# Performance work log

Hardware: AMD Instinct MI355X
Metric: run time of the kernel (lower is better)

## Reference

```python
import jax, jax.numpy as jnp
import numpy as np

N_NODES = 50000
E_DIM = 128
H_DIM = 256
OUT_DIM = 2
N_EDGES = 800000
NEG_SLOPE = 0.01  # nn.LeakyReLU default


def gcn_conv(x, W, b, src, dst, n):
    """PyG GCNConv: h = x @ W; add self-loops; sym-normalized scatter-add; + bias."""
    h = x @ W  # [N, H]
    loop = jnp.arange(n, dtype=src.dtype)
    s = jnp.concatenate([src, loop])
    d = jnp.concatenate([dst, loop])
    w = jnp.ones_like(s, dtype=h.dtype)
    deg = jax.ops.segment_sum(w, d, num_segments=n)  # in-degree incl. self-loop
    dis = jnp.where(deg > 0, jax.lax.rsqrt(deg), jnp.zeros_like(deg))
    norm = dis[s] * dis[d]  # [E+N]
    msg = h[s] * norm[:, None]  # gather + scale
    out = jax.ops.segment_sum(msg, d, num_segments=n)  # scatter-add to targets
    return out + b


def setup_inputs() -> dict:
    key = jax.random.key(0)
    ks = jax.random.split(key, 12)
    inp = {
        "mask_feature": jax.random.normal(ks[0], (N_NODES, E_DIM), jnp.float32),
        "feature": jax.random.normal(ks[1], (N_NODES, E_DIM), jnp.float32),
        "edge_index": jax.random.randint(ks[2], (2, N_EDGES), 0, N_NODES, jnp.int64 if jax.config.jax_enable_x64 else jnp.int32),
        "edge_type": jax.random.randint(ks[3], (N_EDGES,), 0, 2, jnp.int64 if jax.config.jax_enable_x64 else jnp.int32),
        # learned parameters
        "W_in": jax.random.normal(ks[4], (E_DIM, H_DIM), jnp.float32) * 0.05,
        "b_in": jnp.zeros((H_DIM,), jnp.float32),
        "Wg1": jax.random.normal(ks[5], (H_DIM, H_DIM), jnp.float32) * 0.05,
        "bg1": jnp.zeros((H_DIM,), jnp.float32),
        "Wg2": jax.random.normal(ks[6], (H_DIM, H_DIM), jnp.float32) * 0.05,
        "bg2": jnp.zeros((H_DIM,), jnp.float32),
        "W_out": jax.random.normal(ks[7], (H_DIM, OUT_DIM), jnp.float32) * 0.05,
        "b_out": jnp.zeros((OUT_DIM,), jnp.float32),
    }
    return inp


def reference(mask_feature, feature, edge_index, edge_type,
              W_in, b_in, Wg1, bg1, Wg2, bg2, W_out, b_out):
    src, dst = edge_index[0], edge_index[1]
    n = mask_feature.shape[0]
    # main branch
    x = jax.nn.leaky_relu(mask_feature @ W_in + b_in, NEG_SLOPE)
    x = gcn_conv(x, Wg1, bg1, src, dst, n)
    # dropout is identity at inference
    x = gcn_conv(x, Wg2, bg2, src, dst, n)
    x = x @ W_out + b_out  # [N, out_dim]
    # mask branch
    m = jax.nn.leaky_relu((feature - mask_feature) @ W_in + b_in, NEG_SLOPE)
    m = m @ W_out + b_out  # [N, out_dim]
    return x * m
```

## Files before the change

kernel.cpp:

```cpp
#include <hip/hip_runtime.h>


#define NEG_SLOPE 0.01f
constexpr int HD = 256;
constexpr int CHUNK = 4096;
constexpr int BSTRIDE = 8192;

typedef __bf16 bf16x8 __attribute__((ext_vector_type(8)));
typedef unsigned short u16x8 __attribute__((ext_vector_type(8)));
typedef float f32x4 __attribute__((ext_vector_type(4)));

#define MFMA16 __builtin_amdgcn_mfma_f32_16x16x32_bf16

__device__ inline void split1(float v, unsigned short& h, unsigned short& l) {
  unsigned u = __float_as_uint(v);
  unsigned hb = u & 0xFFFF0000u;
  float lf = v - __uint_as_float(hb);
  unsigned ul = __float_as_uint(lf);
  h = (unsigned short)(hb >> 16);
  l = (unsigned short)((ul + 0x7FFFu + ((ul >> 16) & 1u)) >> 16);
}

__global__ __launch_bounds__(256) void k_prep(
    const float* __restrict__ Win, u16x8* __restrict__ Wf,
    const float* __restrict__ Wg1, const float* __restrict__ Wg2,
    const float* __restrict__ Wo, const float* __restrict__ bg1,
    const float* __restrict__ bg2, const float* __restrict__ bo,
    float* __restrict__ wb, float* __restrict__ uv, int* __restrict__ cur) {
  __shared__ float wt[256][2];
  const int bid = blockIdx.x, tid = threadIdx.x;
  if (bid < 32) {
    int f = bid * 4 + (tid >> 6);
    int lane = tid & 63;
    int nt = f >> 3, ks = (f >> 1) & 3, hl = f & 1;
    int n = nt * 16 + (lane & 15);
    int k0 = ks * 32 + (lane >> 4) * 8;
    u16x8 outv;
    #pragma unroll
    for (int j = 0; j < 8; ++j) {
      unsigned short h, l;
      split1(Win[(size_t)(k0 + j) * HD + n], h, l);
      outv[j] = hl ? l : h;
    }
    Wf[f * 64 + lane] = outv;
  } else if (bid == 32) {
    int r = tid;
    float s0 = 0.f, s1 = 0.f;
    for (int k = 0; k < 256; ++k) {
      float w = Wg2[r * 256 + k];
      s0 = fmaf(w, Wo[k * 2 + 0], s0);
      s1 = fmaf(w, Wo[k * 2 + 1], s1);
    }
    wt[r][0] = s0; wt[r][1] = s1;
    __syncthreads();
    float b0 = 0.f, b1 = 0.f;
    for (int k = 0; k < 256; ++k) {
      float w = Wg1[r * 256 + k];
      b0 = fmaf(w, wt[k][0], b0);
      b1 = fmaf(w, wt[k][1], b1);
    }
    wb[r * 2 + 0] = b0; wb[r * 2 + 1] = b1;
    if (r < 2) {
      float u = 0.f, v = 0.f;
      for (int k = 0; k < 256; ++k) {
        u = fmaf(bg1[k], wt[k][r], u);
        v = fmaf(bg2[k], Wo[k * 2 + r], v);
      }
      uv[r] = u;
      uv[2 + r] = v + bo[r];
    }
  } else {
    cur[tid] = 0;
  }
}

__global__ __launch_bounds__(256) void k_scatter(
    const int* __restrict__ src, const int* __restrict__ dst,
    int* __restrict__ cur, unsigned* __restrict__ packed, int E) {
  __shared__ int bins[256], lstart[256], gbase[256], lcur[256];
  __shared__ int wsum[4];
  __shared__ unsigned sbuf[CHUNK];
  const int t = threadIdx.x, b = blockIdx.x;
  const int lane = t & 63, wid = t >> 6;
  bins[t] = 0;
  __syncthreads();
  const int e0 = b * CHUNK, e1 = min(e0 + CHUNK, E), m = e1 - e0;
  for (int e = e0 + t; e < e1; e += 256)
    atomicAdd(&bins[dst[e] >> 8], 1);
  __syncthreads();
  {
    int v = bins[t], incl = v;
    #pragma unroll
    for (int o = 1; o < 64; o <<= 1) {
      int tmp = __shfl_up(incl, o, 64);
      if (lane >= o) incl += tmp;
    }
    if (lane == 63) wsum[wid] = incl;
    __syncthreads();
    int woff = 0;
    for (int w = 0; w < wid; ++w) woff += wsum[w];
    int st = woff + incl - v;
    lstart[t] = st;
    lcur[t] = st;
    gbase[t] = v ? atomicAdd(&cur[t], v) : 0;
  }
  __syncthreads();
  for (int e = e0 + t; e < e1; e += 256) {
    int d = dst[e], s = src[e];
    int slot = atomicAdd(&lcur[d >> 8], 1);
    sbuf[slot] = ((unsigned)d << 16) | (unsigned)s;
  }
  __syncthreads();
  for (int i = t; i < m; i += 256) {
    unsigned pv = sbuf[i];
    int bin = pv >> 24;
    packed[(size_t)bin * BSTRIDE + gbase[bin] + (i - lstart[bin])] = pv;
  }
}

__global__ __launch_bounds__(256) void k_p2(
    const unsigned* __restrict__ packed, const int* __restrict__ cur,
    int* __restrict__ rp, float4* __restrict__ q, int* __restrict__ csr, int N) {
  __shared__ int cnt[256], sc[256];
  __shared__ int wsum[4];
  __shared__ unsigned short sbuf[BSTRIDE];
  const int t = threadIdx.x;
  const int B = blockIdx.x;
  const int lane = t & 63, wid = t >> 6;
  int tot = cur[t], incl = tot;
  #pragma unroll
  for (int o = 1; o < 64; o <<= 1) {
    int tmp = __shfl_up(incl, o, 64);
    if (lane >= o) incl += tmp;
  }
  if (lane == 63) wsum[wid] = incl;
  __syncthreads();
  int woff = 0;
  for (int w = 0; w < wid; ++w) woff += wsum[w];
  sc[t] = woff + incl - tot;
  __syncthreads();
  const int base = sc[B];
  const int ecnt = cur[B];
  const unsigned* pk = packed + (size_t)B * BSTRIDE;
  cnt[t] = 0;
  __syncthreads();
  for (int i = t; i < ecnt; i += 256)
    atomicAdd(&cnt[(pk[i] >> 16) & 0xFF], 1);
  __syncthreads();
  int v = cnt[t];
  incl = v;
  #pragma unroll
  for (int o = 1; o < 64; o <<= 1) {
    int tmp = __shfl_up(incl, o, 64);
    if (lane >= o) incl += tmp;
  }
  if (lane == 63) wsum[wid] = incl;
  __syncthreads();
  woff = 0;
  for (int w = 0; w < wid; ++w) woff += wsum[w];
  const int off = woff + incl - v;
  const int node = B * 256 + t;
  if (node < N) {
    rp[node] = base + off;
    ((float*)&q[node])[0] = rsqrtf((float)(v + 1));
  } else if (node == N) {
    rp[N] = base + off;
  }
  __syncthreads();
  cnt[t] = off;
  __syncthreads();
  for (int i = t; i < ecnt; i += 256) {
    unsigned pv = pk[i];
    int slot = atomicAdd(&cnt[(pv >> 16) & 0xFF], 1);
    sbuf[slot] = (unsigned short)(pv & 0xFFFFu);
  }
  __syncthreads();
  for (int i = t; i < ecnt; i += 256)
    csr[base + i] = (int)sbuf[i];
}

__global__ __launch_bounds__(512, 2) void k_gemm(
    const float* __restrict__ mf, const float* __restrict__ fe,
    const u16x8* __restrict__ Wf, const float* __restrict__ bi,
    const float* __restrict__ wb, const float* __restrict__ Wo,
    const float* __restrict__ bo, float4* __restrict__ q,
    float* __restrict__ Pm, int M) {
  __shared__ u16x8 sWf[8192];
  const int tid = threadIdx.x;
  #pragma unroll
  for (int i = 0; i < 16; ++i) sWf[tid + i * 512] = Wf[tid + i * 512];
  const int lane = tid & 63, wid = tid >> 6;
  const int base = blockIdx.x * 256 + wid * 32;
  const int kb = (lane >> 4) * 8;

  bf16x8 ahi[2][4], alo[2][4], mhi[2][4], mlo[2][4];
  #pragma unroll
  for (int h = 0; h < 2; ++h) {
    int arow = base + h * 16 + (lane & 15);
    if (arow >= M) arow = M - 1;
    const float* ap = mf + (size_t)arow * 128 + kb;
    const float* fp = fe + (size_t)arow * 128 + kb;
    #pragma unroll
    for (int ks = 0; ks < 4; ++ks) {
      float x[8], y[8];
      *(float4*)&x[0] = *(const float4*)(ap + ks * 32);
      *(float4*)&x[4] = *(const float4*)(ap + ks * 32 + 4);
      *(float4*)&y[0] = *(const float4*)(fp + ks * 32);
      *(float4*)&y[4] = *(const float4*)(fp + ks * 32 + 4);
      u16x8 hA, lA, hM, lM;
      #pragma unroll
      for (int j = 0; j < 8; ++j) {
        unsigned short hh, ll;
        split1(x[j], hh, ll);        hA[j] = hh; lA[j] = ll;
        split1(y[j] - x[j], hh, ll); hM[j] = hh; lM[j] = ll;
      }
      ahi[h][ks] = __builtin_bit_cast(bf16x8, hA);
      alo[h][ks] = __builtin_bit_cast(bf16x8, lA);
      mhi[h][ks] = __builtin_bit_cast(bf16x8, hM);
      mlo[h][ks] = __builtin_bit_cast(bf16x8, lM);
    }
  }
  __syncthreads();

  float s0[2][4] = {}, s1[2][4] = {}, t0[2][4] = {}, t1[2][4] = {};
  #pragma unroll 1
  for (int nt = 0; nt < 16; ++nt) {
    f32x4 aM[2] = {{0,0,0,0},{0,0,0,0}}, aK[2] = {{0,0,0,0},{0,0,0,0}};
    #pragma unroll
    for (int ks = 0; ks < 4; ++ks) {
      bf16x8 bh = __builtin_bit_cast(bf16x8, sWf[(nt * 8 + ks * 2 + 0) * 64 + lane]);
      bf16x8 bl = __builtin_bit_cast(bf16x8, sWf[(nt * 8 + ks * 2 + 1) * 64 + lane]);
      #pragma unroll
      for (int h = 0; h < 2; ++h) {
        aM[h] = MFMA16(ahi[h][ks], bh, aM[h], 0, 0, 0);
        aM[h] = MFMA16(alo[h][ks], bh, aM[h], 0, 0, 0);
        aM[h] = MFMA16(ahi[h][ks], bl, aM[h], 0, 0, 0);
        aK[h] = MFMA16(mhi[h][ks], bh, aK[h], 0, 0, 0);
        aK[h] = MFMA16(mlo[h][ks], bh, aK[h], 0, 0, 0);
        aK[h] = MFMA16(mhi[h][ks], bl, aK[h], 0, 0, 0);
      }
    }
    const int col = nt * 16 + (lane & 15);
    const float bc = bi[col];
    const float w0 = wb[col * 2 + 0], w1 = wb[col * 2 + 1];
    const float v0 = Wo[col * 2 + 0], v1 = Wo[col * 2 + 1];
    #pragma unroll
    for (int h = 0; h < 2; ++h) {
      #pragma unroll
      for (int r = 0; r < 4; ++r) {
        float a = aM[h][r] + bc; a = a > 0.f ? a : NEG_SLOPE * a;
        s0[h][r] = fmaf(a, w0, s0[h][r]); s1[h][r] = fmaf(a, w1, s1[h][r]);
        float m = aK[h][r] + bc; m = m > 0.f ? m : NEG_SLOPE * m;
        t0[h][r] = fmaf(m, v0, t0[h][r]); t1[h][r] = fmaf(m, v1, t1[h][r]);
      }
    }
  }

  #pragma unroll
  for (int o = 1; o < 16; o <<= 1) {
    #pragma unroll
    for (int h = 0; h < 2; ++h) {
      #pragma unroll
      for (int r = 0; r < 4; ++r) {
        s0[h][r] += __shfl_xor(s0[h][r], o, 16);
        s1[h][r] += __shfl_xor(s1[h][r], o, 16);
        t0[h][r] += __shfl_xor(t0[h][r], o, 16);
        t1[h][r] += __shfl_xor(t1[h][r], o, 16);
      }
    }
  }
  if ((lane & 15) == 0) {
    float bo0 = bo[0], bo1 = bo[1];
    #pragma unroll
    for (int h = 0; h < 2; ++h) {
      #pragma unroll
      for (int r = 0; r < 4; ++r) {
        int row = base + h * 16 + (lane >> 4) * 4 + r;
        if (row < M) {
          float* qf = (float*)&q[row];
          qf[1] = s0[h][r];
          qf[2] = s1[h][r];
          Pm[row * 2 + 0] = t0[h][r] + bo0;
          Pm[row * 2 + 1] = t1[h][r] + bo1;
        }
      }
    }
  }
}

__global__ __launch_bounds__(256) void k_gather1(
    const int* __restrict__ rp, const int* __restrict__ csr,
    const float4* __restrict__ q, const float* __restrict__ uv,
    float* __restrict__ T2, int N) {
  int t = threadIdx.x;
  int n = blockIdx.x * 64 + (t >> 2);
  int l = t & 3;
  if (n >= N) return;
  int s0 = rp[n], s1 = rp[n + 1];
  float a0 = 0.f, a1 = 0.f;
  int j = s0 + l;
  for (; j + 4 < s1; j += 8) {
    int sa = csr[j], sb = csr[j + 4];
    float4 qa = q[sa], qb = q[sb];
    a0 = fmaf(qa.x, qa.y, a0); a1 = fmaf(qa.x, qa.z, a1);
    a0 = fmaf(qb.x, qb.y, a0); a1 = fmaf(qb.x, qb.z, a1);
  }
  if (j < s1) {
    float4 qa = q[csr[j]];
    a0 = fmaf(qa.x, qa.y, a0); a1 = fmaf(qa.x, qa.z, a1);
  }
  a0 += __shfl_xor(a0, 1, 4); a1 += __shfl_xor(a1, 1, 4);
  a0 += __shfl_xor(a0, 2, 4); a1 += __shfl_xor(a1, 2, 4);
  if (l == 0) {
    float4 qn = q[n];
    float d = qn.x;
    T2[n * 2 + 0] = d * (d * fmaf(d, qn.y, a0) + uv[0]);
    T2[n * 2 + 1] = d * (d * fmaf(d, qn.z, a1) + uv[1]);
  }
}

__global__ __launch_bounds__(256) void k_gather2(
    const int* __restrict__ rp, const int* __restrict__ csr,
    const float* __restrict__ T2, const float4* __restrict__ q,
    const float* __restrict__ uv, const float* __restrict__ Pm,
    float* __restrict__ out, int N) {
  int t = threadIdx.x;
  int n = blockIdx.x * 64 + (t >> 2);
  int l = t & 3;
  if (n >= N) return;
  int s0 = rp[n], s1 = rp[n + 1];
  float a0 = 0.f, a1 = 0.f;
  int j = s0 + l;
  for (; j + 4 < s1; j += 8) {
    int sa = csr[j], sb = csr[j + 4];
    float2 va = *(const float2*)&T2[sa * 2];
    float2 vb = *(const float2*)&T2[sb * 2];
    a0 += va.x + vb.x; a1 += va.y + vb.y;
  }
  if (j < s1) {
    float2 va = *(const float2*)&T2[csr[j] * 2];
    a0 += va.x; a1 += va.y;
  }
  a0 += __shfl_xor(a0, 1, 4); a1 += __shfl_xor(a1, 1, 4);
  a0 += __shfl_xor(a0, 2, 4); a1 += __shfl_xor(a1, 2, 4);
  if (l == 0) {
    float d = q[n].x;
    float2 tv = *(const float2*)&T2[n * 2];
    float z0 = d * (tv.x + a0) + uv[2];
    float z1 = d * (tv.y + a1) + uv[3];
    out[n * 2 + 0] = z0 * Pm[n * 2 + 0];
    out[n * 2 + 1] = z1 * Pm[n * 2 + 1];
  }
}

extern "C" void kernel_launch(void* const* d_in, const int* in_sizes, int n_in,
                              void* d_out, int out_size, void* d_ws, size_t ws_size,
                              hipStream_t stream) {
  const float* mf  = (const float*)d_in[0];
  const float* fe  = (const float*)d_in[1];
  const int*   ei  = (const int*)d_in[2];
  const float* Win = (const float*)d_in[4];
  const float* bin = (const float*)d_in[5];
  const float* Wg1 = (const float*)d_in[6];
  const float* bg1 = (const float*)d_in[7];
  const float* Wg2 = (const float*)d_in[8];
  const float* bg2 = (const float*)d_in[9];
  const float* Wo  = (const float*)d_in[10];
  const float* bo  = (const float*)d_in[11];
  float* out = (float*)d_out;

  const int ED = 128;
  const int N = in_sizes[0] / ED;
  const int E = in_sizes[3];
  const int* src = ei;
  const int* dst = ei + E;

  char* ws = (char*)d_ws;
  size_t off = 0;
  auto carve = [&](size_t bytes) {
    char* p = ws + off;
    off += (bytes + 255) & ~(size_t)255;
    return p;
  };
  int*      cur    = (int*)carve(256 * 4);
  unsigned* packed = (unsigned*)carve((size_t)256 * BSTRIDE * 4);
  int*      csr    = (int*)carve((size_t)E * 4);
  int*      rp     = (int*)carve((size_t)(N + 1) * 4);
  float4*   q      = (float4*)carve((size_t)N * 16);
  float*    T2     = (float*)carve((size_t)N * 2 * 4);
  float*    Pm     = (float*)carve((size_t)N * 2 * 4);
  float*    wb     = (float*)carve((size_t)HD * 2 * 4);
  float*    uv     = (float*)carve(4 * 4);
  u16x8*    Wf     = (u16x8*)carve((size_t)128 * 64 * 16);
  (void)ws_size; (void)n_in; (void)out_size;

  const int NB  = (E + CHUNK - 1) / CHUNK;
  const int NP2 = (N + 255) / 256;
  const int Gg  = (N + 255) / 256;
  const int Gt  = (N + 63) / 64;

  k_prep<<<34, 256, 0, stream>>>(Win, Wf, Wg1, Wg2, Wo, bg1, bg2, bo, wb, uv, cur);
  k_scatter<<<NB, 256, 0, stream>>>(src, dst, cur, packed, E);
  k_p2<<<NP2, 256, 0, stream>>>(packed, cur, rp, q, csr, N);
  k_gemm<<<Gg, 512, 0, stream>>>(mf, fe, Wf, bin, wb, Wo, bo, q, Pm, N);
  k_gather1<<<Gt, 256, 0, stream>>>(rp, csr, q, uv, T2, N);
  k_gather2<<<Gt, 256, 0, stream>>>(rp, csr, T2, q, uv, Pm, out, N);
}
```

Before: 100.8 us.

## Fuse CSR build and GEMM into one launch, stream weights in chunks, unroll gathers

Result: faster. 89.54 us (-11.2%).

```diff
diff --git a/kernel.cpp b/kernel.cpp
--- a/kernel.cpp
+++ b/kernel.cpp
@@ -118,88 +118,32 @@
   }
 }
 
-__global__ __launch_bounds__(256) void k_p2(
-    const unsigned* __restrict__ packed, const int* __restrict__ cur,
-    int* __restrict__ rp, float4* __restrict__ q, int* __restrict__ csr, int N) {
-  __shared__ int cnt[256], sc[256];
-  __shared__ int wsum[4];
-  __shared__ unsigned short sbuf[BSTRIDE];
-  const int t = threadIdx.x;
-  const int B = blockIdx.x;
-  const int lane = t & 63, wid = t >> 6;
-  int tot = cur[t], incl = tot;
-  #pragma unroll
-  for (int o = 1; o < 64; o <<= 1) {
-    int tmp = __shfl_up(incl, o, 64);
-    if (lane >= o) incl += tmp;
-  }
-  if (lane == 63) wsum[wid] = incl;
-  __syncthreads();
-  int woff = 0;
-  for (int w = 0; w < wid; ++w) woff += wsum[w];
-  sc[t] = woff + incl - tot;
-  __syncthreads();
-  const int base = sc[B];
-  const int ecnt = cur[B];
-  const unsigned* pk = packed + (size_t)B * BSTRIDE;
-  cnt[t] = 0;
-  __syncthreads();
-  for (int i = t; i < ecnt; i += 256)
-    atomicAdd(&cnt[(pk[i] >> 16) & 0xFF], 1);
-  __syncthreads();
-  int v = cnt[t];
-  incl = v;
-  #pragma unroll
-  for (int o = 1; o < 64; o <<= 1) {
-    int tmp = __shfl_up(incl, o, 64);
-    if (lane >= o) incl += tmp;
-  }
-  if (lane == 63) wsum[wid] = incl;
-  __syncthreads();
-  woff = 0;
-  for (int w = 0; w < wid; ++w) woff += wsum[w];
-  const int off = woff + incl - v;
-  const int node = B * 256 + t;
-  if (node < N) {
-    rp[node] = base + off;
-    ((float*)&q[node])[0] = rsqrtf((float)(v + 1));
-  } else if (node == N) {
-    rp[N] = base + off;
-  }
-  __syncthreads();
-  cnt[t] = off;
-  __syncthreads();
-  for (int i = t; i < ecnt; i += 256) {
-    unsigned pv = pk[i];
-    int slot = atomicAdd(&cnt[(pv >> 16) & 0xFF], 1);
-    sbuf[slot] = (unsigned short)(pv & 0xFFFFu);
-  }
-  __syncthreads();
-  for (int i = t; i < ecnt; i += 256)
-    csr[base + i] = (int)sbuf[i];
-}
-
-__global__ __launch_bounds__(512, 2) void k_gemm(
+__global__ __launch_bounds__(256, 3) void k_main(
     const float* __restrict__ mf, const float* __restrict__ fe,
     const u16x8* __restrict__ Wf, const float* __restrict__ bi,
     const float* __restrict__ wb, const float* __restrict__ Wo,
-    const float* __restrict__ bo, float4* __restrict__ q,
-    float* __restrict__ Pm, int M) {
-  __shared__ u16x8 sWf[8192];
+    const float* __restrict__ bo, float4* __restrict__ q, float* __restrict__ Pm,
+    const unsigned* __restrict__ packed, const int* __restrict__ cur,
+    int* __restrict__ rp, int* __restrict__ csr, int N, int Gg) {
+  __shared__ __align__(16) char smem[38912];
   const int tid = threadIdx.x;
-  #pragma unroll
-  for (int i = 0; i < 16; ++i) sWf[tid + i * 512] = Wf[tid + i * 512];
   const int lane = tid & 63, wid = tid >> 6;
-  const int base = blockIdx.x * 256 + wid * 32;
-  const int kb = (lane >> 4) * 8;
-
-  bf16x8 ahi[2][4], alo[2][4], mhi[2][4], mlo[2][4];
-  #pragma unroll
-  for (int h = 0; h < 2; ++h) {
-    int arow = base + h * 16 + (lane & 15);
-    if (arow >= M) arow = M - 1;
+
+  if ((int)blockIdx.x < Gg) {
+    u16x8*  sB  = (u16x8*)smem;
+    float4* sE1 = (float4*)(smem + 32768);
+    float2* sE2 = (float2*)(smem + 36864);
+    sE1[tid] = make_float4(bi[tid], wb[2 * tid], wb[2 * tid + 1], 0.f);
+    sE2[tid] = make_float2(Wo[2 * tid], Wo[2 * tid + 1]);
+
+    const int base = blockIdx.x * 64 + wid * 16;
+    int arow = base + (lane & 15);
+    if (arow >= N) arow = N - 1;
+    const int kb = (lane >> 4) * 8;
     const float* ap = mf + (size_t)arow * 128 + kb;
     const float* fp = fe + (size_t)arow * 128 + kb;
+
+    bf16x8 ahi[4], alo[4], mhi[4], mlo[4];
     #pragma unroll
     for (int ks = 0; ks < 4; ++ks) {
       float x[8], y[8];
@@ -214,78 +158,129 @@
         split1(x[j], hh, ll);        hA[j] = hh; lA[j] = ll;
         split1(y[j] - x[j], hh, ll); hM[j] = hh; lM[j] = ll;
       }
-      ahi[h][ks] = __builtin_bit_cast(bf16x8, hA);
-      alo[h][ks] = __builtin_bit_cast(bf16x8, lA);
-      mhi[h][ks] = __builtin_bit_cast(bf16x8, hM);
-      mlo[h][ks] = __builtin_bit_cast(bf16x8, lM);
-    }
-  }
-  __syncthreads();
-
-  float s0[2][4] = {}, s1[2][4] = {}, t0[2][4] = {}, t1[2][4] = {};
-  #pragma unroll 1
-  for (int nt = 0; nt < 16; ++nt) {
-    f32x4 aM[2] = {{0,0,0,0},{0,0,0,0}}, aK[2] = {{0,0,0,0},{0,0,0,0}};
+      ahi[ks] = __builtin_bit_cast(bf16x8, hA);
+      alo[ks] = __builtin_bit_cast(bf16x8, lA);
+      mhi[ks] = __builtin_bit_cast(bf16x8, hM);
+      mlo[ks] = __builtin_bit_cast(bf16x8, lM);
+    }
+
+    float s0[4] = {}, s1[4] = {}, t0[4] = {}, t1[4] = {};
+    #pragma unroll 1
+    for (int g = 0; g < 4; ++g) {
+      __syncthreads();
+      #pragma unroll
+      for (int i = 0; i < 8; ++i)
+        sB[tid + i * 256] = Wf[g * 2048 + tid + i * 256];
+      __syncthreads();
+      #pragma unroll
+      for (int ntl = 0; ntl < 4; ++ntl) {
+        const int nt = g * 4 + ntl;
+        f32x4 aM = {0, 0, 0, 0}, aK = {0, 0, 0, 0};
+        #pragma unroll
+        for (int ks = 0; ks < 4; ++ks) {
+          bf16x8 bh = __builtin_bit_cast(bf16x8, sB[(ntl * 8 + ks * 2 + 0) * 64 + lane]);
+          bf16x8 bl = __builtin_bit_cast(bf16x8, sB[(ntl * 8 + ks * 2 + 1) * 64 + lane]);
+          aM = MFMA16(ahi[ks], bh, aM, 0, 0, 0);
+          aM = MFMA16(alo[ks], bh, aM, 0, 0, 0);
+          aM = MFMA16(ahi[ks], bl, aM, 0, 0, 0);
+          aK = MFMA16(mhi[ks], bh, aK, 0, 0, 0);
+          aK = MFMA16(mlo[ks], bh, aK, 0, 0, 0);
+          aK = MFMA16(mhi[ks], bl, aK, 0, 0, 0);
+        }
+        const int col = nt * 16 + (lane & 15);
+        const float4 e1 = sE1[col];
+        const float2 e2 = sE2[col];
+        #pragma unroll
+        for (int r = 0; r < 4; ++r) {
+          float a = aM[r] + e1.x; a = a > 0.f ? a : NEG_SLOPE * a;
+          s0[r] = fmaf(a, e1.y, s0[r]); s1[r] = fmaf(a, e1.z, s1[r]);
+          float m = aK[r] + e1.x; m = m > 0.f ? m : NEG_SLOPE * m;
+          t0[r] = fmaf(m, e2.x, t0[r]); t1[r] = fmaf(m, e2.y, t1[r]);
+        }
+      }
+    }
+
     #pragma unroll
-    for (int ks = 0; ks < 4; ++ks) {
-      bf16x8 bh = __builtin_bit_cast(bf16x8, sWf[(nt * 8 + ks * 2 + 0) * 64 + lane]);
-      bf16x8 bl = __builtin_bit_cast(bf16x8, sWf[(nt * 8 + ks * 2 + 1) * 64 + lane]);
-      #pragma unroll
-      for (int h = 0; h < 2; ++h) {
-        aM[h] = MFMA16(ahi[h][ks], bh, aM[h], 0, 0, 0);
-        aM[h] = MFMA16(alo[h][ks], bh, aM[h], 0, 0, 0);
-        aM[h] = MFMA16(ahi[h][ks], bl, aM[h], 0, 0, 0);
-        aK[h] = MFMA16(mhi[h][ks], bh, aK[h], 0, 0, 0);
-        aK[h] = MFMA16(mlo[h][ks], bh, aK[h], 0, 0, 0);
-        aK[h] = MFMA16(mhi[h][ks], bl, aK[h], 0, 0, 0);
-      }
-    }
-    const int col = nt * 16 + (lane & 15);
-    const float bc = bi[col];
-    const float w0 = wb[col * 2 + 0], w1 = wb[col * 2 + 1];
-    const float v0 = Wo[col * 2 + 0], v1 = Wo[col * 2 + 1];
-    #pragma unroll
-    for (int h = 0; h < 2; ++h) {
+    for (int o = 1; o < 16; o <<= 1) {
       #pragma unroll
       for (int r = 0; r < 4; ++r) {
-        float a = aM[h][r] + bc; a = a > 0.f ? a : NEG_SLOPE * a;
-        s0[h][r] = fmaf(a, w0, s0[h][r]); s1[h][r] = fmaf(a, w1, s1[h][r]);
-        float m = aK[h][r] + bc; m = m > 0.f ? m : NEG_SLOPE * m;
-        t0[h][r] = fmaf(m, v0, t0[h][r]); t1[h][r] = fmaf(m, v1, t1[h][r]);
+        s0[r] += __shfl_xor(s0[r], o, 16); s1[r] += __shfl_xor(s1[r], o, 16);
+        t0[r] += __shfl_xor(t0[r], o, 16); t1[r] += __shfl_xor(t1[r], o, 16);
       }
     }
-  }
-
-  #pragma unroll
-  for (int o = 1; o < 16; o <<= 1) {
-    #pragma unroll
-    for (int h = 0; h < 2; ++h) {
+    if ((lane & 15) == 0) {
+      float bo0 = bo[0], bo1 = bo[1];
       #pragma unroll
       for (int r = 0; r < 4; ++r) {
-        s0[h][r] += __shfl_xor(s0[h][r], o, 16);
-        s1[h][r] += __shfl_xor(s1[h][r], o, 16);
-        t0[h][r] += __shfl_xor(t0[h][r], o, 16);
-        t1[h][r] += __shfl_xor(t1[h][r], o, 16);
-      }
-    }
-  }
-  if ((lane & 15) == 0) {
-    float bo0 = bo[0], bo1 = bo[1];
-    #pragma unroll
-    for (int h = 0; h < 2; ++h) {
-      #pragma unroll
-      for (int r = 0; r < 4; ++r) {
-        int row = base + h * 16 + (lane >> 4) * 4 + r;
-        if (row < M) {
+        int row = base + (lane >> 4) * 4 + r;
+        if (row < N) {
           float* qf = (float*)&q[row];
-          qf[1] = s0[h][r];
-          qf[2] = s1[h][r];
-          Pm[row * 2 + 0] = t0[h][r] + bo0;
-          Pm[row * 2 + 1] = t1[h][r] + bo1;
+          qf[1] = s0[r];
+          qf[2] = s1[r];
+          Pm[row * 2 + 0] = t0[r] + bo0;
+          Pm[row * 2 + 1] = t1[r] + bo1;
         }
       }
     }
-  }
+    return;
+  }
+
+  int* cnt = (int*)smem;
+  int* sc  = (int*)(smem + 1024);
+  int* wsum = (int*)(smem + 2048);
+  unsigned short* sbuf = (unsigned short*)(smem + 2064);
+  const int t = tid;
+  const int B = blockIdx.x - Gg;
+  int tot = cur[t], incl = tot;
+  #pragma unroll
+  for (int o = 1; o < 64; o <<= 1) {
+    int tmp = __shfl_up(incl, o, 64);
+    if (lane >= o) incl += tmp;
+  }
+  if (lane == 63) wsum[wid] = incl;
+  __syncthreads();
+  int woff = 0;
+  for (int w = 0; w < wid; ++w) woff += wsum[w];
+  sc[t] = woff + incl - tot;
+  __syncthreads();
+  const int base = sc[B];
+  const int ecnt = cur[B];
+  const unsigned* pk = packed + (size_t)B * BSTRIDE;
+  cnt[t] = 0;
+  __syncthreads();
+  for (int i = t; i < ecnt; i += 256)
+    atomicAdd(&cnt[(pk[i] >> 16) & 0xFF], 1);
+  __syncthreads();
+  int v = cnt[t];
+  incl = v;
+  #pragma unroll
+  for (int o = 1; o < 64; o <<= 1) {
+    int tmp = __shfl_up(incl, o, 64);
+    if (lane >= o) incl += tmp;
+  }
+  if (lane == 63) wsum[wid] = incl;
+  __syncthreads();
+  woff = 0;
+  for (int w = 0; w < wid; ++w) woff += wsum[w];
+  const int off = woff + incl - v;
+  const int node = B * 256 + t;
+  if (node < N) {
+    rp[node] = base + off;
+    ((float*)&q[node])[0] = rsqrtf((float)(v + 1));
+  } else if (node == N) {
+    rp[N] = base + off;
+  }
+  __syncthreads();
+  cnt[t] = off;
+  __syncthreads();
+  for (int i = t; i < ecnt; i += 256) {
+    unsigned pv = pk[i];
+    int slot = atomicAdd(&cnt[(pv >> 16) & 0xFF], 1);
+    sbuf[slot] = (unsigned short)(pv & 0xFFFFu);
+  }
+  __syncthreads();
+  for (int i = t; i < ecnt; i += 256)
+    csr[base + i] = (int)sbuf[i];
 }
 
 __global__ __launch_bounds__(256) void k_gather1(
@@ -299,13 +294,15 @@
   int s0 = rp[n], s1 = rp[n + 1];
   float a0 = 0.f, a1 = 0.f;
   int j = s0 + l;
-  for (; j + 4 < s1; j += 8) {
-    int sa = csr[j], sb = csr[j + 4];
-    float4 qa = q[sa], qb = q[sb];
-    a0 = fmaf(qa.x, qa.y, a0); a1 = fmaf(qa.x, qa.z, a1);
-    a0 = fmaf(qb.x, qb.y, a0); a1 = fmaf(qb.x, qb.z, a1);
-  }
-  if (j < s1) {
+  for (; j + 12 < s1; j += 16) {
+    int i0 = csr[j], i1 = csr[j + 4], i2 = csr[j + 8], i3 = csr[j + 12];
+    float4 q0 = q[i0], q1 = q[i1], q2 = q[i2], q3 = q[i3];
+    a0 = fmaf(q0.x, q0.y, a0); a1 = fmaf(q0.x, q0.z, a1);
+    a0 = fmaf(q1.x, q1.y, a0); a1 = fmaf(q1.x, q1.z, a1);
+    a0 = fmaf(q2.x, q2.y, a0); a1 = fmaf(q2.x, q2.z, a1);
+    a0 = fmaf(q3.x, q3.y, a0); a1 = fmaf(q3.x, q3.z, a1);
+  }
+  for (; j < s1; j += 4) {
     float4 qa = q[csr[j]];
     a0 = fmaf(qa.x, qa.y, a0); a1 = fmaf(qa.x, qa.z, a1);
   }
@@ -331,13 +328,16 @@
   int s0 = rp[n], s1 = rp[n + 1];
   float a0 = 0.f, a1 = 0.f;
   int j = s0 + l;
-  for (; j + 4 < s1; j += 8) {
-    int sa = csr[j], sb = csr[j + 4];
-    float2 va = *(const float2*)&T2[sa * 2];
-    float2 vb = *(const float2*)&T2[sb * 2];
-    a0 += va.x + vb.x; a1 += va.y + vb.y;
-  }
-  if (j < s1) {
+  for (; j + 12 < s1; j += 16) {
+    int i0 = csr[j], i1 = csr[j + 4], i2 = csr[j + 8], i3 = csr[j + 12];
+    float2 v0 = *(const float2*)&T2[i0 * 2];
+    float2 v1 = *(const float2*)&T2[i1 * 2];
+    float2 v2 = *(const float2*)&T2[i2 * 2];
+    float2 v3 = *(const float2*)&T2[i3 * 2];
+    a0 += (v0.x + v1.x) + (v2.x + v3.x);
+    a1 += (v0.y + v1.y) + (v2.y + v3.y);
+  }
+  for (; j < s1; j += 4) {
     float2 va = *(const float2*)&T2[csr[j] * 2];
     a0 += va.x; a1 += va.y;
   }
@@ -396,13 +396,13 @@
 
   const int NB  = (E + CHUNK - 1) / CHUNK;
   const int NP2 = (N + 255) / 256;
-  const int Gg  = (N + 255) / 256;
+  const int Gg  = (N + 63) / 64;
   const int Gt  = (N + 63) / 64;
 
   k_prep<<<34, 256, 0, stream>>>(Win, Wf, Wg1, Wg2, Wo, bg1, bg2, bo, wb, uv, cur);
   k_scatter<<<NB, 256, 0, stream>>>(src, dst, cur, packed, E);
-  k_p2<<<NP2, 256, 0, stream>>>(packed, cur, rp, q, csr, N);
-  k_gemm<<<Gg, 512, 0, stream>>>(mf, fe, Wf, bin, wb, Wo, bo, q, Pm, N);
+  k_main<<<Gg + NP2, 256, 0, stream>>>(mf, fe, Wf, bin, wb, Wo, bo, q, Pm,
+                                       packed, cur, rp, csr, N, Gg);
   k_gather1<<<Gt, 256, 0, stream>>>(rp, csr, q, uv, T2, N);
   k_gather2<<<Gt, 256, 0, stream>>>(rp, csr, T2, q, uv, Pm, out, N);
 }
```
